# Kernel tuning notes

Hardware: AMD Instinct MI355X
Metric: run time of the kernel (lower is better)

Reference implementation:

```python
import jax, jax.numpy as jnp
import numpy as np

ATTN_HEAD = 8

def setup_inputs() -> dict:
    key = jax.random.key(0)
    ks = jax.random.split(key, 5)
    nf, nloc, nnei, fd = 4, 2048, 64, 256
    query = jax.random.normal(ks[0], (nf, nloc, fd), dtype=jnp.float32)
    attn_bias = jax.random.normal(ks[1], (nf, ATTN_HEAD, nloc, nnei), dtype=jnp.float32)
    nlist = jax.random.randint(ks[2], (nf, nloc, nnei), 0, nloc, dtype=jnp.int64)
    nlist_mask = jnp.ones((nf, nloc, nnei), dtype=bool)
    # in_proj params: matrix (fd, 3fd), bias (1, 3fd), init per SimpleLinear
    W = jax.random.normal(ks[3], (fd, 3 * fd), dtype=jnp.float32) / np.sqrt(fd + 3 * fd)
    b = jax.random.normal(ks[4], (1, 3 * fd), dtype=jnp.float32)
    return {"query": query, "attn_bias": attn_bias, "nlist_mask": nlist_mask,
            "nlist": nlist, "W": W, "b": b}

def reference(query, attn_bias, nlist_mask, nlist, W, b):
    nf, nloc, fd = query.shape
    H = ATTN_HEAD
    hd = fd // H
    nnei = nlist.shape[-1]
    scaling = float(hd) ** -0.5
    qkv = query @ W + b                      # (nf, nloc, 3*fd)
    q, k, v = jnp.split(qkv, 3, axis=-1)
    q = q.reshape(nf, nloc, H, hd) * scaling # (nf, nloc, H, hd)
    idx = nlist.reshape(nf, nloc * nnei)[..., None]  # gather along atom axis
    kg = jnp.take_along_axis(k, idx, axis=1).reshape(nf, nloc, nnei, H, hd)
    vg = jnp.take_along_axis(v, idx, axis=1).reshape(nf, nloc, nnei, H, hd)
    aw = jnp.einsum('blhd,blnhd->bhln', q, kg)       # (nf, H, nloc, nnei)
    aw = jnp.where(nlist_mask[:, None, :, :], aw, -jnp.inf)
    aw = aw + attn_bias                              # return_attn=True path
    attn = jax.nn.softmax(aw, axis=-1)
    o = jnp.einsum('bhln,blnhd->blhd', attn, vg).reshape(nf, nloc, fd)
    return o, aw, attn.reshape(nf * H * nloc, 1, nnei)
```

## Files before the change

### kernel.cpp

```cpp
#include <hip/hip_runtime.h>
#include <hip/hip_bf16.h>

#define NF    4
#define NLOC  2048
#define FD    256
#define NH    8
#define HD    32
#define NNEI  64
#define N3    (3*FD)
#define MTOT  (NF*NLOC)

typedef __attribute__((ext_vector_type(2))) float          f32x2;
typedef __attribute__((ext_vector_type(8))) short          bf16x8;
typedef __attribute__((ext_vector_type(4))) float          f32x4;
typedef __attribute__((ext_vector_type(8))) unsigned short u16x8;
typedef __attribute__((ext_vector_type(2))) _Float16       h16x2;

__device__ __forceinline__ f32x2 upk2(unsigned int u) {
    f32x2 r;
    r.x = __uint_as_float(u << 16);
    r.y = __uint_as_float(u & 0xffff0000u);
    return r;
}
__device__ __forceinline__ h16x2 as_h2(unsigned int u) {
    return __builtin_bit_cast(h16x2, u);
}
__device__ __forceinline__ h16x2 pkrtz(float a, float b) {
    return __builtin_bit_cast(h16x2, __builtin_amdgcn_cvt_pkrtz(a, b));
}
__device__ __forceinline__ unsigned short f2b(float x) {
    __hip_bfloat16 h = __float2bfloat16(x);
    return __builtin_bit_cast(unsigned short, h);
}
__device__ __forceinline__ unsigned short f2h(float x) {
    return __builtin_bit_cast(unsigned short, (_Float16)x);
}
__device__ __forceinline__ u16x8 cvt8(float4 a, float4 b) {
    u16x8 o;
    o[0] = f2b(a.x); o[1] = f2b(a.y); o[2] = f2b(a.z); o[3] = f2b(a.w);
    o[4] = f2b(b.x); o[5] = f2b(b.y); o[6] = f2b(b.z); o[7] = f2b(b.w);
    return o;
}

__global__ __launch_bounds__(256) void convT_w_kernel(
    const float* __restrict__ Wm, unsigned short* __restrict__ Wt)
{
    __shared__ float tile[32][33];
    const int t  = threadIdx.x;
    const int tx = t & 31;
    const int ty = t >> 5;
    const int bx = blockIdx.x;
    const int by = blockIdx.y;
    #pragma unroll
    for (int i = 0; i < 4; ++i) {
        const int kk = ty + i * 8;
        tile[kk][tx] = Wm[(size_t)(by * 32 + kk) * N3 + bx * 32 + tx];
    }
    __syncthreads();
    #pragma unroll
    for (int i = 0; i < 4; ++i) {
        const int nn = ty + i * 8;
        Wt[(size_t)(bx * 32 + nn) * FD + by * 32 + tx] = f2b(tile[tx][nn]);
    }
}

#define LDA 40

__global__ __launch_bounds__(256) void qkv_gemm_mfma(
    const float* __restrict__ query,
    const unsigned short* __restrict__ Wt,
    const float* __restrict__ bv,
    float* __restrict__ qw,
    unsigned short* __restrict__ kw16,
    unsigned short* __restrict__ vw16,
    float scaling)
{
    __shared__ unsigned short As[128 * LDA];
    __shared__ unsigned short Bs[64 * LDA];

    const int t  = threadIdx.x;
    const int bm = blockIdx.x;
    const int bn = blockIdx.y;
    const int l  = t & 63;
    const int w  = t >> 6;
    const int wm = w >> 1;
    const int wn = w & 1;

    const int srow = t >> 2;
    const int scol = (t & 3) * 8;

    const float* Aq = query + (size_t)(bm * 128) * FD;
    const unsigned short* Bq = Wt + (size_t)(bn * 64) * FD;

    f32x4 acc[4][2] = {};

    float4 pa0 = *reinterpret_cast<const float4*>(Aq + (size_t)srow * FD + scol);
    float4 pa1 = *reinterpret_cast<const float4*>(Aq + (size_t)srow * FD + scol + 4);
    float4 pb0 = *reinterpret_cast<const float4*>(Aq + (size_t)(srow + 64) * FD + scol);
    float4 pb1 = *reinterpret_cast<const float4*>(Aq + (size_t)(srow + 64) * FD + scol + 4);
    u16x8 rb0  = *reinterpret_cast<const u16x8*>(Bq + (size_t)srow * FD + scol);

    for (int k0 = 0; k0 < FD; k0 += 32) {
        __syncthreads();
        *reinterpret_cast<u16x8*>(As + srow * LDA + scol)        = cvt8(pa0, pa1);
        *reinterpret_cast<u16x8*>(As + (srow + 64) * LDA + scol) = cvt8(pb0, pb1);
        *reinterpret_cast<u16x8*>(Bs + srow * LDA + scol)        = rb0;
        __syncthreads();

        if (k0 + 32 < FD) {
            pa0 = *reinterpret_cast<const float4*>(Aq + (size_t)srow * FD + k0 + 32 + scol);
            pa1 = *reinterpret_cast<const float4*>(Aq + (size_t)srow * FD + k0 + 32 + scol + 4);
            pb0 = *reinterpret_cast<const float4*>(Aq + (size_t)(srow + 64) * FD + k0 + 32 + scol);
            pb1 = *reinterpret_cast<const float4*>(Aq + (size_t)(srow + 64) * FD + k0 + 32 + scol + 4);
            rb0 = *reinterpret_cast<const u16x8*>(Bq + (size_t)srow * FD + k0 + 32 + scol);
        }

        const int kq = (l >> 4) * 8;
        bf16x8 af[4], bfr[2];
        #pragma unroll
        for (int i = 0; i < 4; ++i)
            af[i] = *reinterpret_cast<const bf16x8*>(As + (wm * 64 + i * 16 + (l & 15)) * LDA + kq);
        #pragma unroll
        for (int j = 0; j < 2; ++j)
            bfr[j] = *reinterpret_cast<const bf16x8*>(Bs + (wn * 32 + j * 16 + (l & 15)) * LDA + kq);
        #pragma unroll
        for (int i = 0; i < 4; ++i)
            #pragma unroll
            for (int j = 0; j < 2; ++j)
                acc[i][j] = __builtin_amdgcn_mfma_f32_16x16x32_bf16(af[i], bfr[j], acc[i][j], 0, 0, 0);
    }

    const int kind = bn >> 2;
    #pragma unroll
    for (int j = 0; j < 2; ++j) {
        const int ncol = bn * 64 + wn * 32 + j * 16 + (l & 15);
        const float bb = bv[ncol];
        const int cm = ncol & (FD - 1);
        #pragma unroll
        for (int i = 0; i < 4; ++i) {
            const int mrow = bm * 128 + wm * 64 + i * 16 + (l >> 4) * 4;
            #pragma unroll
            for (int r = 0; r < 4; ++r) {
                const float val = acc[i][j][r] + bb;
                const size_t off = (size_t)(mrow + r) * FD + cm;
                if (kind == 0)      qw[off]   = val * scaling;
                else if (kind == 1) kw16[off] = f2h(val);
                else                vw16[off] = f2b(val);
            }
        }
    }
}

__global__ __launch_bounds__(256) void attn_kernel(
    const float* __restrict__ qw,
    const unsigned short* __restrict__ kw16,
    const unsigned short* __restrict__ vw16,
    const float* __restrict__ bias,
    const int*   __restrict__ nlist,
    float* __restrict__ o_out,
    float* __restrict__ aw_out,
    float* __restrict__ attn_out)
{
    const int blk = blockIdx.x;
    const int xcd = blk & 7;
    const int f   = xcd >> 1;
    const int l   = ((xcd & 1) << 10) + (blk >> 3);
    const int bl  = f * NLOC + l;

    const int t  = threadIdx.x;
    const int hp = t >> 6;
    const int ln = t & 63;
    const int hs = ln >> 5;
    const int g  = (ln >> 2) & 7;
    const int od = ln & 3;
    const int h  = hp * 2 + hs;

    const int idxv = nlist[(size_t)bl * NNEI + ln];

    const float* qp = qw + (size_t)bl * FD + h * HD + od * 8;
    const float4 qa = *reinterpret_cast<const float4*>(qp);
    const float4 qb = *reinterpret_cast<const float4*>(qp + 4);

    const size_t base_h = (((size_t)f * NH + h) * NLOC + l) * NNEI;

    int nid[8];
    #pragma unroll
    for (int k = 0; k < 8; ++k)
        nid[k] = __shfl(idxv, 8 * k + g);

    float bb[8];
    #pragma unroll
    for (int k = 0; k < 8; ++k)
        bb[k] = bias[base_h + 8 * k + g];

    const unsigned short* kf = kw16 + (size_t)f * NLOC * FD + h * HD + od * 8;
    const unsigned short* vf = vw16 + (size_t)f * NLOC * FD + h * HD + od * 8;

    uint4 kr[8];
    #pragma unroll
    for (int k = 0; k < 8; ++k)
        kr[k] = *reinterpret_cast<const uint4*>(kf + (size_t)nid[k] * FD);

    uint4 vr[8];
    #pragma unroll
    for (int k = 0; k < 8; ++k)
        vr[k] = *reinterpret_cast<const uint4*>(vf + (size_t)nid[k] * FD);

    __builtin_amdgcn_sched_barrier(0);

    h16x2 qh[4];
    qh[0] = pkrtz(qa.x, qa.y);
    qh[1] = pkrtz(qa.z, qa.w);
    qh[2] = pkrtz(qb.x, qb.y);
    qh[3] = pkrtz(qb.z, qb.w);

    float s[8];
    #pragma unroll
    for (int k = 0; k < 8; ++k) {
        float ps = 0.f;
        ps = __builtin_amdgcn_fdot2(as_h2(kr[k].x), qh[0], ps, false);
        ps = __builtin_amdgcn_fdot2(as_h2(kr[k].y), qh[1], ps, false);
        ps = __builtin_amdgcn_fdot2(as_h2(kr[k].z), qh[2], ps, false);
        ps = __builtin_amdgcn_fdot2(as_h2(kr[k].w), qh[3], ps, false);
        ps += __shfl_xor(ps, 1);
        ps += __shfl_xor(ps, 2);
        s[k] = ps + bb[k];
    }

    float m = fmaxf(fmaxf(fmaxf(s[0], s[1]), fmaxf(s[2], s[3])),
                    fmaxf(fmaxf(s[4], s[5]), fmaxf(s[6], s[7])));
    m = fmaxf(m, __shfl_xor(m, 4));
    m = fmaxf(m, __shfl_xor(m, 8));
    m = fmaxf(m, __shfl_xor(m, 16));

    float e[8];
    float S = 0.f;
    #pragma unroll
    for (int k = 0; k < 8; ++k) {
        e[k] = __expf(s[k] - m);
        S += e[k];
    }
    S += __shfl_xor(S, 4);
    S += __shfl_xor(S, 8);
    S += __shfl_xor(S, 16);
    const float rinv = __builtin_amdgcn_rcpf(S);

    float p[8];
    #pragma unroll
    for (int k = 0; k < 8; ++k) p[k] = e[k] * rinv;

    aw_out[base_h + 8 * od + g]        = s[od];
    aw_out[base_h + 8 * (od + 4) + g]  = s[od + 4];
    attn_out[base_h + 8 * od + g]       = p[od];
    attn_out[base_h + 8 * (od + 4) + g] = p[od + 4];

    f32x2 acc[4] = {};
    #pragma unroll
    for (int k = 0; k < 8; ++k) {
        f32x2 pb; pb.x = p[k]; pb.y = p[k];
        acc[0] += upk2(vr[k].x) * pb;
        acc[1] += upk2(vr[k].y) * pb;
        acc[2] += upk2(vr[k].z) * pb;
        acc[3] += upk2(vr[k].w) * pb;
    }
    #pragma unroll
    for (int c = 0; c < 4; ++c) {
        acc[c].x += __shfl_xor(acc[c].x, 4);
        acc[c].y += __shfl_xor(acc[c].y, 4);
        acc[c].x += __shfl_xor(acc[c].x, 8);
        acc[c].y += __shfl_xor(acc[c].y, 8);
        acc[c].x += __shfl_xor(acc[c].x, 16);
        acc[c].y += __shfl_xor(acc[c].y, 16);
    }
    if (g == 0) {
        float* op = o_out + (size_t)bl * FD + h * HD + od * 8;
        *reinterpret_cast<float4*>(op)     = make_float4(acc[0].x, acc[0].y, acc[1].x, acc[1].y);
        *reinterpret_cast<float4*>(op + 4) = make_float4(acc[2].x, acc[2].y, acc[3].x, acc[3].y);
    }
}

extern "C" void kernel_launch(void* const* d_in, const int* in_sizes, int n_in,
                              void* d_out, int out_size, void* d_ws, size_t ws_size,
                              hipStream_t stream) {
    const float* query = (const float*)d_in[0];
    const float* bias  = (const float*)d_in[1];
    const int*   nlist = (const int*)d_in[3];
    const float* Wm    = (const float*)d_in[4];
    const float* bv    = (const float*)d_in[5];

    float* out      = (float*)d_out;
    float* o_out    = out;
    float* aw_out   = out + (size_t)NF * NLOC * FD;
    float* attn_out = aw_out + (size_t)NF * NH * NLOC * NNEI;

    float*          qw   = (float*)d_ws;
    unsigned short* kw16 = (unsigned short*)(qw + (size_t)MTOT * FD);
    unsigned short* vw16 = kw16 + (size_t)MTOT * FD;
    unsigned short* Wt   = vw16 + (size_t)MTOT * FD;

    const float scaling = 0.17677669529663687f;

    convT_w_kernel<<<dim3(N3 / 32, FD / 32), 256, 0, stream>>>(Wm, Wt);
    qkv_gemm_mfma<<<dim3(MTOT / 128, N3 / 64), 256, 0, stream>>>(query, Wt, bv, qw, kw16, vw16, scaling);
    attn_kernel<<<MTOT, 256, 0, stream>>>(qw, kw16, vw16, bias, nlist, o_out, aw_out, attn_out);
}
```

Measured before the change: 54.83 us.

## Hand-schedule gather loads with inline asm and remap neighbors per lane

Each lane group now owns 8 contiguous neighbors, so it loads nlist and bias directly as dwordx4 instead of broadcasting indices with shuffles. All K and V gathers are issued through inline asm global_load instructions using scalar bases. Explicit vmcnt waits let the score and softmax math start while the V loads are still in flight. The aw and attn writes become float4 stores from one lane per group. The aim is to cut shuffles and scalar stores and to hide gather latency, at the cost of brittle hand-written asm ordering and fewer lanes doing the stores.

```diff
diff --git a/kernel.cpp b/kernel.cpp
--- a/kernel.cpp
+++ b/kernel.cpp
@@ -15,6 +15,8 @@
 typedef __attribute__((ext_vector_type(4))) float          f32x4;
 typedef __attribute__((ext_vector_type(8))) unsigned short u16x8;
 typedef __attribute__((ext_vector_type(2))) _Float16       h16x2;
+typedef __attribute__((ext_vector_type(4))) int            i32x4;
+typedef __attribute__((ext_vector_type(4))) unsigned int   u32x4;
 
 __device__ __forceinline__ f32x2 upk2(unsigned int u) {
     f32x2 r;
@@ -175,57 +177,80 @@
     const int od = ln & 3;
     const int h  = hp * 2 + hs;
 
-    const int idxv = nlist[(size_t)bl * NNEI + ln];
-
-    const float* qp = qw + (size_t)bl * FD + h * HD + od * 8;
-    const float4 qa = *reinterpret_cast<const float4*>(qp);
-    const float4 qb = *reinterpret_cast<const float4*>(qp + 4);
-
-    const size_t base_h = (((size_t)f * NH + h) * NLOC + l) * NNEI;
-
-    int nid[8];
-    #pragma unroll
-    for (int k = 0; k < 8; ++k)
-        nid[k] = __shfl(idxv, 8 * k + g);
-
-    float bb[8];
-    #pragma unroll
-    for (int k = 0; k < 8; ++k)
-        bb[k] = bias[base_h + 8 * k + g];
-
-    const unsigned short* kf = kw16 + (size_t)f * NLOC * FD + h * HD + od * 8;
-    const unsigned short* vf = vw16 + (size_t)f * NLOC * FD + h * HD + od * 8;
-
-    uint4 kr[8];
-    #pragma unroll
-    for (int k = 0; k < 8; ++k)
-        kr[k] = *reinterpret_cast<const uint4*>(kf + (size_t)nid[k] * FD);
-
-    uint4 vr[8];
-    #pragma unroll
-    for (int k = 0; k < 8; ++k)
-        vr[k] = *reinterpret_cast<const uint4*>(vf + (size_t)nid[k] * FD);
-
+    const unsigned nl_off = ((unsigned)(bl * NNEI + 8 * g)) << 2;
+    const unsigned q_off  = ((unsigned)(bl * FD + h * HD + od * 8)) << 2;
+    const size_t  base_h  = (((size_t)f * NH + h) * NLOC + l) * NNEI;
+    const unsigned b_off  = ((unsigned)base_h + 8u * g) << 2;
+
+    i32x4 n0, n1; f32x4 q0, q1, b0, b1;
+    asm volatile("global_load_dwordx4 %0, %1, %2"           : "=v"(n0) : "v"(nl_off), "s"(nlist));
+    asm volatile("global_load_dwordx4 %0, %1, %2 offset:16" : "=v"(n1) : "v"(nl_off), "s"(nlist));
+    asm volatile("global_load_dwordx4 %0, %1, %2"           : "=v"(q0) : "v"(q_off),  "s"(qw));
+    asm volatile("global_load_dwordx4 %0, %1, %2 offset:16" : "=v"(q1) : "v"(q_off),  "s"(qw));
+    asm volatile("global_load_dwordx4 %0, %1, %2"           : "=v"(b0) : "v"(b_off),  "s"(bias));
+    asm volatile("global_load_dwordx4 %0, %1, %2 offset:16" : "=v"(b1) : "v"(b_off),  "s"(bias));
+
+    asm volatile("s_waitcnt vmcnt(4)" : "+v"(n0), "+v"(n1));
     __builtin_amdgcn_sched_barrier(0);
 
-    h16x2 qh[4];
-    qh[0] = pkrtz(qa.x, qa.y);
-    qh[1] = pkrtz(qa.z, qa.w);
-    qh[2] = pkrtz(qb.x, qb.y);
-    qh[3] = pkrtz(qb.z, qb.w);
+    const unsigned dim2 = ((unsigned)(h * HD + od * 8)) << 1;
+    const unsigned short* kf = kw16 + (size_t)f * NLOC * FD;
+    const unsigned short* vf = vw16 + (size_t)f * NLOC * FD;
+
+    const unsigned ko0 = ((unsigned)n0[0] << 9) + dim2;
+    const unsigned ko1 = ((unsigned)n0[1] << 9) + dim2;
+    const unsigned ko2 = ((unsigned)n0[2] << 9) + dim2;
+    const unsigned ko3 = ((unsigned)n0[3] << 9) + dim2;
+    const unsigned ko4 = ((unsigned)n1[0] << 9) + dim2;
+    const unsigned ko5 = ((unsigned)n1[1] << 9) + dim2;
+    const unsigned ko6 = ((unsigned)n1[2] << 9) + dim2;
+    const unsigned ko7 = ((unsigned)n1[3] << 9) + dim2;
+
+    u32x4 kr0, kr1, kr2, kr3, kr4, kr5, kr6, kr7;
+    u32x4 vr0, vr1, vr2, vr3, vr4, vr5, vr6, vr7;
+    asm volatile("global_load_dwordx4 %0, %1, %2" : "=v"(kr0) : "v"(ko0), "s"(kf));
+    asm volatile("global_load_dwordx4 %0, %1, %2" : "=v"(kr1) : "v"(ko1), "s"(kf));
+    asm volatile("global_load_dwordx4 %0, %1, %2" : "=v"(kr2) : "v"(ko2), "s"(kf));
+    asm volatile("global_load_dwordx4 %0, %1, %2" : "=v"(kr3) : "v"(ko3), "s"(kf));
+    asm volatile("global_load_dwordx4 %0, %1, %2" : "=v"(kr4) : "v"(ko4), "s"(kf));
+    asm volatile("global_load_dwordx4 %0, %1, %2" : "=v"(kr5) : "v"(ko5), "s"(kf));
+    asm volatile("global_load_dwordx4 %0, %1, %2" : "=v"(kr6) : "v"(ko6), "s"(kf));
+    asm volatile("global_load_dwordx4 %0, %1, %2" : "=v"(kr7) : "v"(ko7), "s"(kf));
+    asm volatile("global_load_dwordx4 %0, %1, %2" : "=v"(vr0) : "v"(ko0), "s"(vf));
+    asm volatile("global_load_dwordx4 %0, %1, %2" : "=v"(vr1) : "v"(ko1), "s"(vf));
+    asm volatile("global_load_dwordx4 %0, %1, %2" : "=v"(vr2) : "v"(ko2), "s"(vf));
+    asm volatile("global_load_dwordx4 %0, %1, %2" : "=v"(vr3) : "v"(ko3), "s"(vf));
+    asm volatile("global_load_dwordx4 %0, %1, %2" : "=v"(vr4) : "v"(ko4), "s"(vf));
+    asm volatile("global_load_dwordx4 %0, %1, %2" : "=v"(vr5) : "v"(ko5), "s"(vf));
+    asm volatile("global_load_dwordx4 %0, %1, %2" : "=v"(vr6) : "v"(ko6), "s"(vf));
+    asm volatile("global_load_dwordx4 %0, %1, %2" : "=v"(vr7) : "v"(ko7), "s"(vf));
+
+    asm volatile("s_waitcnt vmcnt(8)"
+        : "+v"(q0), "+v"(q1), "+v"(b0), "+v"(b1),
+          "+v"(kr0), "+v"(kr1), "+v"(kr2), "+v"(kr3),
+          "+v"(kr4), "+v"(kr5), "+v"(kr6), "+v"(kr7));
+    __builtin_amdgcn_sched_barrier(0);
+
+    const h16x2 qh0 = pkrtz(q0[0], q0[1]);
+    const h16x2 qh1 = pkrtz(q0[2], q0[3]);
+    const h16x2 qh2 = pkrtz(q1[0], q1[1]);
+    const h16x2 qh3 = pkrtz(q1[2], q1[3]);
+
+    const float bb[8] = {b0[0], b0[1], b0[2], b0[3], b1[0], b1[1], b1[2], b1[3]};
 
     float s[8];
-    #pragma unroll
-    for (int k = 0; k < 8; ++k) {
-        float ps = 0.f;
-        ps = __builtin_amdgcn_fdot2(as_h2(kr[k].x), qh[0], ps, false);
-        ps = __builtin_amdgcn_fdot2(as_h2(kr[k].y), qh[1], ps, false);
-        ps = __builtin_amdgcn_fdot2(as_h2(kr[k].z), qh[2], ps, false);
-        ps = __builtin_amdgcn_fdot2(as_h2(kr[k].w), qh[3], ps, false);
-        ps += __shfl_xor(ps, 1);
-        ps += __shfl_xor(ps, 2);
-        s[k] = ps + bb[k];
-    }
+#define SCORE(i, KR) do {                                              \
+        float ps = __builtin_amdgcn_fdot2(as_h2(KR[0]), qh0, 0.f, false); \
+        ps = __builtin_amdgcn_fdot2(as_h2(KR[1]), qh1, ps, false);     \
+        ps = __builtin_amdgcn_fdot2(as_h2(KR[2]), qh2, ps, false);     \
+        ps = __builtin_amdgcn_fdot2(as_h2(KR[3]), qh3, ps, false);     \
+        ps += __shfl_xor(ps, 1);                                       \
+        ps += __shfl_xor(ps, 2);                                       \
+        s[i] = ps + bb[i];                                             \
+    } while (0)
+    SCORE(0, kr0); SCORE(1, kr1); SCORE(2, kr2); SCORE(3, kr3);
+    SCORE(4, kr4); SCORE(5, kr5); SCORE(6, kr6); SCORE(7, kr7);
+#undef SCORE
 
     float m = fmaxf(fmaxf(fmaxf(s[0], s[1]), fmaxf(s[2], s[3])),
                     fmaxf(fmaxf(s[4], s[5]), fmaxf(s[6], s[7])));
@@ -249,33 +274,51 @@
     #pragma unroll
     for (int k = 0; k < 8; ++k) p[k] = e[k] * rinv;
 
-    aw_out[base_h + 8 * od + g]        = s[od];
-    aw_out[base_h + 8 * (od + 4) + g]  = s[od + 4];
-    attn_out[base_h + 8 * od + g]       = p[od];
-    attn_out[base_h + 8 * (od + 4) + g] = p[od + 4];
-
-    f32x2 acc[4] = {};
-    #pragma unroll
-    for (int k = 0; k < 8; ++k) {
-        f32x2 pb; pb.x = p[k]; pb.y = p[k];
-        acc[0] += upk2(vr[k].x) * pb;
-        acc[1] += upk2(vr[k].y) * pb;
-        acc[2] += upk2(vr[k].z) * pb;
-        acc[3] += upk2(vr[k].w) * pb;
-    }
-    #pragma unroll
-    for (int c = 0; c < 4; ++c) {
-        acc[c].x += __shfl_xor(acc[c].x, 4);
-        acc[c].y += __shfl_xor(acc[c].y, 4);
-        acc[c].x += __shfl_xor(acc[c].x, 8);
-        acc[c].y += __shfl_xor(acc[c].y, 8);
-        acc[c].x += __shfl_xor(acc[c].x, 16);
-        acc[c].y += __shfl_xor(acc[c].y, 16);
-    }
+    asm volatile("s_waitcnt vmcnt(0)"
+        : "+v"(vr0), "+v"(vr1), "+v"(vr2), "+v"(vr3),
+          "+v"(vr4), "+v"(vr5), "+v"(vr6), "+v"(vr7));
+    __builtin_amdgcn_sched_barrier(0);
+
+    if (od == 0) {
+        *reinterpret_cast<float4*>(aw_out + base_h + 8 * g) =
+            make_float4(s[0], s[1], s[2], s[3]);
+        *reinterpret_cast<float4*>(aw_out + base_h + 8 * g + 4) =
+            make_float4(s[4], s[5], s[6], s[7]);
+        *reinterpret_cast<float4*>(attn_out + base_h + 8 * g) =
+            make_float4(p[0], p[1], p[2], p[3]);
+        *reinterpret_cast<float4*>(attn_out + base_h + 8 * g + 4) =
+            make_float4(p[4], p[5], p[6], p[7]);
+    }
+
+    f32x2 acc0 = {0.f, 0.f}, acc1 = {0.f, 0.f}, acc2 = {0.f, 0.f}, acc3 = {0.f, 0.f};
+#define PV(i, VR) do {                        \
+        f32x2 pb; pb.x = p[i]; pb.y = p[i];   \
+        acc0 += upk2(VR[0]) * pb;             \
+        acc1 += upk2(VR[1]) * pb;             \
+        acc2 += upk2(VR[2]) * pb;             \
+        acc3 += upk2(VR[3]) * pb;             \
+    } while (0)
+    PV(0, vr0); PV(1, vr1); PV(2, vr2); PV(3, vr3);
+    PV(4, vr4); PV(5, vr5); PV(6, vr6); PV(7, vr7);
+#undef PV
+
+    acc0.x += __shfl_xor(acc0.x, 4);  acc0.y += __shfl_xor(acc0.y, 4);
+    acc1.x += __shfl_xor(acc1.x, 4);  acc1.y += __shfl_xor(acc1.y, 4);
+    acc2.x += __shfl_xor(acc2.x, 4);  acc2.y += __shfl_xor(acc2.y, 4);
+    acc3.x += __shfl_xor(acc3.x, 4);  acc3.y += __shfl_xor(acc3.y, 4);
+    acc0.x += __shfl_xor(acc0.x, 8);  acc0.y += __shfl_xor(acc0.y, 8);
+    acc1.x += __shfl_xor(acc1.x, 8);  acc1.y += __shfl_xor(acc1.y, 8);
+    acc2.x += __shfl_xor(acc2.x, 8);  acc2.y += __shfl_xor(acc2.y, 8);
+    acc3.x += __shfl_xor(acc3.x, 8);  acc3.y += __shfl_xor(acc3.y, 8);
+    acc0.x += __shfl_xor(acc0.x, 16); acc0.y += __shfl_xor(acc0.y, 16);
+    acc1.x += __shfl_xor(acc1.x, 16); acc1.y += __shfl_xor(acc1.y, 16);
+    acc2.x += __shfl_xor(acc2.x, 16); acc2.y += __shfl_xor(acc2.y, 16);
+    acc3.x += __shfl_xor(acc3.x, 16); acc3.y += __shfl_xor(acc3.y, 16);
+
     if (g == 0) {
         float* op = o_out + (size_t)bl * FD + h * HD + od * 8;
-        *reinterpret_cast<float4*>(op)     = make_float4(acc[0].x, acc[0].y, acc[1].x, acc[1].y);
-        *reinterpret_cast<float4*>(op + 4) = make_float4(acc[2].x, acc[2].y, acc[3].x, acc[3].y);
+        *reinterpret_cast<float4*>(op)     = make_float4(acc0.x, acc0.y, acc1.x, acc1.y);
+        *reinterpret_cast<float4*>(op + 4) = make_float4(acc2.x, acc2.y, acc3.x, acc3.y);
     }
 }
 
```

Result: no change. 55.05 us (+0.4%).
